# Kernel optimization log

Measured on AMD Instinct MI355X. Metric: run time of the kernel, lower is better.

## Reference

```python
import jax, jax.numpy as jnp
import numpy as np

N_NODES = 262144
D_IN = 256
EMBED_DIM = 256
BATCH_SIZE = 64  # hardcoded in the original module


def setup_inputs() -> dict:
    key = jax.random.key(0)
    k1, k2, k3, k4, k5, k6, k7 = jax.random.split(key, 7)
    nodes = jax.random.normal(k1, (N_NODES, D_IN), dtype=jnp.float32)
    indicator = jnp.sort(jax.random.randint(k2, (N_NODES,), 0, BATCH_SIZE)).astype(jnp.int64)
    mask = jax.random.uniform(k3, (N_NODES,), dtype=jnp.float32)
    # Dense layer params (glorot-like scale)
    scale = 1.0 / np.sqrt(D_IN)
    Wg = jax.random.normal(k4, (D_IN, EMBED_DIM), dtype=jnp.float32) * scale
    bg = jnp.zeros((EMBED_DIM,), dtype=jnp.float32)
    Wf = jax.random.normal(k5, (D_IN, EMBED_DIM), dtype=jnp.float32) * scale
    bf = jnp.zeros((EMBED_DIM,), dtype=jnp.float32)
    return {"nodes": nodes, "indicator": indicator, "mask": mask,
            "Wg": Wg, "bg": bg, "Wf": Wf, "bf": bf}


def reference(nodes, indicator, mask, Wg, bg, Wf, bf):
    seg = indicator.astype(jnp.int32)
    m = mask[:, None]                                   # [N, 1]
    gate = jax.nn.sigmoid(nodes @ Wg + bg)              # [N, E]
    feat = jnp.tanh(nodes @ Wf + bf)                    # [N, E]
    gated_x = gate * feat * m                           # [N, E]
    seg_sum = jax.ops.segment_sum(gated_x, seg, num_segments=BATCH_SIZE)   # [B, E]
    seg_cnt = jax.ops.segment_sum(m, seg, num_segments=BATCH_SIZE)         # [B, 1]
    x_mean = seg_sum / jnp.maximum(seg_cnt, 1e-6)
    x_max = jax.ops.segment_max(gated_x, seg, num_segments=BATCH_SIZE)     # [B, E]
    return jnp.concatenate([x_mean, x_max], axis=-1)    # [B, 2E]
```

## Files before the change

kernel.cpp:

```cpp
#include <hip/hip_runtime.h>
#include <hip/hip_bf16.h>


#define N_NODES 262144
#define BM 64
#define NBLK (N_NODES / BM)

typedef short bf16x8 __attribute__((ext_vector_type(8)));
typedef float f32x4 __attribute__((ext_vector_type(4)));

#define BT_OFF      0
#define SEG_SUM_OFF 262144
#define SEG_MAX_OFF 327680
#define SEG_CNT_OFF 393216

__device__ __forceinline__ unsigned short f2bf(float x) {
    unsigned u = __float_as_uint(x);
    u += 0x7FFFu + ((u >> 16) & 1u);
    return (unsigned short)(u >> 16);
}

__device__ __forceinline__ void atomicMaxF(float* addr, float v) {
    if (v >= 0.0f) atomicMax((int*)addr, __float_as_int(v));
    else           atomicMin((unsigned int*)addr, __float_as_uint(v));
}

__device__ __forceinline__ float fast_sigmoid(float x) {
    return __builtin_amdgcn_rcpf(1.0f + __builtin_amdgcn_exp2f(-1.4426950408889634f * x));
}
__device__ __forceinline__ float fast_tanh(float x) {
    return 1.0f - 2.0f * __builtin_amdgcn_rcpf(1.0f + __builtin_amdgcn_exp2f(2.8853900817779268f * x));
}

__global__ void gr_init(const float* __restrict__ Wg, const float* __restrict__ Wf,
                        unsigned short* __restrict__ Bt, float* __restrict__ seg_sum,
                        float* __restrict__ seg_max, float* __restrict__ seg_cnt) {
    int tid = blockIdx.x * 256 + threadIdx.x;
    int n = tid >> 8, k = tid & 255;
    float v = (n < 256) ? Wg[k * 256 + n] : Wf[k * 256 + (n - 256)];
    Bt[n * 256 + k] = f2bf(v);
    if (tid < 16384) { seg_sum[tid] = 0.0f; seg_max[tid] = __uint_as_float(0xFF800000u); }
    if (tid < 64) seg_cnt[tid] = 0.0f;
}

__global__ __launch_bounds__(512) void gr_main(
    const float* __restrict__ nodes, const int* __restrict__ indicator,
    const float* __restrict__ mask, const float* __restrict__ bg,
    const float* __restrict__ bfb, const unsigned short* __restrict__ Bt,
    float* __restrict__ seg_sum, float* __restrict__ seg_max, float* __restrict__ seg_cnt)
{
    __shared__ unsigned short sA[64 * 264];
    __shared__ unsigned short sB[512 * 40];
    __shared__ float sMask[64];
    __shared__ int sSeg[64];

    const int t = threadIdx.x;
    const long r0 = (long)blockIdx.x * BM;

    #pragma unroll
    for (int i = 0; i < 4; ++i) {
        int c = t + i * 512;
        int row = c >> 5, g = c & 31;
        const float* src = nodes + (r0 + row) * 256 + g * 8;
        float4 f0 = *(const float4*)(src);
        float4 f1 = *(const float4*)(src + 4);
        union { bf16x8 v; unsigned short u[8]; } w;
        w.u[0] = f2bf(f0.x); w.u[1] = f2bf(f0.y); w.u[2] = f2bf(f0.z); w.u[3] = f2bf(f0.w);
        w.u[4] = f2bf(f1.x); w.u[5] = f2bf(f1.y); w.u[6] = f2bf(f1.z); w.u[7] = f2bf(f1.w);
        *reinterpret_cast<bf16x8*>(&sA[row * 264 + g * 8]) = w.v;
    }
    if (t < 64) { sMask[t] = mask[r0 + t]; sSeg[t] = indicator[r0 + t]; }

    const int lane = t & 63, wid = t >> 6;
    const int wr = wid >> 2, wc = wid & 3;
    const int l15 = lane & 15, l4 = lane >> 4;

    f32x4 acc[2][8];
    #pragma unroll
    for (int f = 0; f < 2; ++f)
        #pragma unroll
        for (int n = 0; n < 8; ++n) acc[f][n] = (f32x4){0.f, 0.f, 0.f, 0.f};

    for (int ks = 0; ks < 8; ++ks) {
        __syncthreads();
        #pragma unroll
        for (int i = 0; i < 4; ++i) {
            int c = t + i * 512;
            int n = c >> 2, g = c & 3;
            *reinterpret_cast<bf16x8*>(&sB[n * 40 + g * 8]) =
                *reinterpret_cast<const bf16x8*>(Bt + n * 256 + ks * 32 + g * 8);
        }
        __syncthreads();
        bf16x8 a0 = *reinterpret_cast<const bf16x8*>(&sA[(wr * 32 + l15) * 264 + ks * 32 + l4 * 8]);
        bf16x8 a1 = *reinterpret_cast<const bf16x8*>(&sA[(wr * 32 + 16 + l15) * 264 + ks * 32 + l4 * 8]);
        #pragma unroll
        for (int n = 0; n < 8; ++n) {
            int col = (n < 4) ? (wc * 64 + n * 16) : (256 + wc * 64 + (n - 4) * 16);
            bf16x8 b = *reinterpret_cast<const bf16x8*>(&sB[(col + l15) * 40 + l4 * 8]);
            acc[0][n] = __builtin_amdgcn_mfma_f32_16x16x32_bf16(a0, b, acc[0][n], 0, 0, 0);
            acc[1][n] = __builtin_amdgcn_mfma_f32_16x16x32_bf16(a1, b, acc[1][n], 0, 0, 0);
        }
    }

    const int strip = wr * 32;
    float gated[2][4][4];
    #pragma unroll
    for (int n = 0; n < 4; ++n) {
        int e = wc * 64 + n * 16 + l15;
        float bgv = bg[e], bfv = bfb[e];
        #pragma unroll
        for (int f = 0; f < 2; ++f)
            #pragma unroll
            for (int i = 0; i < 4; ++i) {
                int row = strip + f * 16 + l4 * 4 + i;
                float g = acc[f][n][i] + bgv;
                float h = acc[f][n + 4][i] + bfv;
                gated[f][n][i] = fast_sigmoid(g) * fast_tanh(h) * sMask[row];
            }
    }

    int seg0 = sSeg[strip], seg1 = sSeg[strip + 31];
    if (seg0 == seg1) {
        #pragma unroll
        for (int n = 0; n < 4; ++n) {
            float s = 0.f, m = -3.4e38f;
            #pragma unroll
            for (int f = 0; f < 2; ++f)
                #pragma unroll
                for (int i = 0; i < 4; ++i) {
                    s += gated[f][n][i];
                    m = fmaxf(m, gated[f][n][i]);
                }
            s += __shfl_xor(s, 16); s += __shfl_xor(s, 32);
            m = fmaxf(m, __shfl_xor(m, 16)); m = fmaxf(m, __shfl_xor(m, 32));
            if (l4 == 0) {
                int e = wc * 64 + n * 16 + l15;
                atomicAdd(&seg_sum[seg0 * 256 + e], s);
                atomicMaxF(&seg_max[seg0 * 256 + e], m);
            }
        }
    } else {
        #pragma unroll
        for (int n = 0; n < 4; ++n) {
            int e = wc * 64 + n * 16 + l15;
            #pragma unroll
            for (int f = 0; f < 2; ++f)
                #pragma unroll
                for (int i = 0; i < 4; ++i) {
                    int row = strip + f * 16 + l4 * 4 + i;
                    int sg = sSeg[row];
                    atomicAdd(&seg_sum[sg * 256 + e], gated[f][n][i]);
                    atomicMaxF(&seg_max[sg * 256 + e], gated[f][n][i]);
                }
        }
    }

    if (wid == 0) {
        float mv = sMask[lane];
        if (sSeg[0] == sSeg[63]) {
            float tot = mv;
            #pragma unroll
            for (int off = 1; off < 64; off <<= 1) tot += __shfl_xor(tot, off);
            if (lane == 0) atomicAdd(&seg_cnt[sSeg[0]], tot);
        } else {
            atomicAdd(&seg_cnt[sSeg[lane]], mv);
        }
    }
}

__global__ void gr_final(const float* __restrict__ seg_sum, const float* __restrict__ seg_max,
                         const float* __restrict__ seg_cnt, float* __restrict__ out) {
    int tid = blockIdx.x * 256 + threadIdx.x;
    int s = tid >> 9, j = tid & 511;
    float r;
    if (j < 256) r = seg_sum[s * 256 + j] / fmaxf(seg_cnt[s], 1e-6f);
    else         r = seg_max[s * 256 + (j - 256)];
    out[tid] = r;
}

extern "C" void kernel_launch(void* const* d_in, const int* in_sizes, int n_in,
                              void* d_out, int out_size, void* d_ws, size_t ws_size,
                              hipStream_t stream) {
    const float* nodes     = (const float*)d_in[0];
    const int*   indicator = (const int*)d_in[1];
    const float* mask      = (const float*)d_in[2];
    const float* Wg        = (const float*)d_in[3];
    const float* bg        = (const float*)d_in[4];
    const float* Wf        = (const float*)d_in[5];
    const float* bf        = (const float*)d_in[6];
    float* out = (float*)d_out;

    unsigned short* Bt = (unsigned short*)((char*)d_ws + BT_OFF);
    float* seg_sum = (float*)((char*)d_ws + SEG_SUM_OFF);
    float* seg_max = (float*)((char*)d_ws + SEG_MAX_OFF);
    float* seg_cnt = (float*)((char*)d_ws + SEG_CNT_OFF);

    gr_init<<<512, 256, 0, stream>>>(Wg, Wf, Bt, seg_sum, seg_max, seg_cnt);
    gr_main<<<NBLK, 512, 0, stream>>>(nodes, indicator, mask, bg, bf, Bt,
                                      seg_sum, seg_max, seg_cnt);
    gr_final<<<128, 256, 0, stream>>>(seg_sum, seg_max, seg_cnt, out);
}
```

Measured before the change: 506.1 us.

## Pre-swizzle weights into MFMA fragment layout and load B directly from global

The init kernel now writes the bf16 weights in a fragment-ready layout, transposing through LDS, so each lane of the main kernel can load its B operand with one 16-byte global load per tile. This removes the per-k-step LDS staging of B and the two barriers around it. Each wave now owns 32 output columns across all 64 rows, using a 4x4 MFMA tile instead of 2x8. Launch bounds request two blocks per CU, and mixed-segment tiles get a per-16-row reduction path. The risk is that every block re-reads the 256 KB of weights from L2 and gets less B reuse.

After: 426.3 us. 1.19x faster.

```diff
diff --git a/kernel.cpp b/kernel.cpp
--- a/kernel.cpp
+++ b/kernel.cpp
@@ -33,24 +33,54 @@
 }
 
 __global__ void gr_init(const float* __restrict__ Wg, const float* __restrict__ Wf,
-                        unsigned short* __restrict__ Bt, float* __restrict__ seg_sum,
+                        unsigned short* __restrict__ Btf, float* __restrict__ seg_sum,
                         float* __restrict__ seg_max, float* __restrict__ seg_cnt) {
-    int tid = blockIdx.x * 256 + threadIdx.x;
-    int n = tid >> 8, k = tid & 255;
-    float v = (n < 256) ? Wg[k * 256 + n] : Wf[k * 256 + (n - 256)];
-    Bt[n * 256 + k] = f2bf(v);
-    if (tid < 16384) { seg_sum[tid] = 0.0f; seg_max[tid] = __uint_as_float(0xFF800000u); }
-    if (tid < 64) seg_cnt[tid] = 0.0f;
-}
-
-__global__ __launch_bounds__(512) void gr_main(
+    int b = blockIdx.x;
+    int t = threadIdx.x;
+    if (b >= 32) {
+        int tid = (b - 32) * 256 + t;
+        for (int i = tid; i < 16384; i += 1024) {
+            seg_sum[i] = 0.0f;
+            seg_max[i] = __uint_as_float(0xFF800000u);
+        }
+        if (tid < 64) seg_cnt[tid] = 0.0f;
+        return;
+    }
+    __shared__ float lds[64][68];
+    const int kt  = b >> 3;
+    const int ct0 = (b & 7) * 64;
+    const float* W = (ct0 < 256) ? Wg : Wf;
+    const int cbase = (ct0 < 256) ? ct0 : ct0 - 256;
+    #pragma unroll
+    for (int p = 0; p < 4; ++p) {
+        int kk = (t >> 4) + p * 16;
+        int cc = (t & 15) * 4;
+        float4 v = *(const float4*)(W + (kt * 64 + kk) * 256 + cbase + cc);
+        lds[kk][cc] = v.x; lds[kk][cc + 1] = v.y; lds[kk][cc + 2] = v.z; lds[kk][cc + 3] = v.w;
+    }
+    __syncthreads();
+    #pragma unroll
+    for (int p = 0; p < 2; ++p) {
+        int g = t + p * 256;
+        int lane = g & 63, ksg = (g >> 6) & 1, ct = g >> 7;
+        int cc = ct * 16 + (lane & 15);
+        int kk = ksg * 32 + (lane >> 4) * 8;
+        union { bf16x8 v; unsigned short u[8]; } w;
+        #pragma unroll
+        for (int j = 0; j < 8; ++j) w.u[j] = f2bf(lds[kk + j][cc]);
+        int gct = (ct0 >> 4) + ct;
+        int ks  = kt * 2 + ksg;
+        *reinterpret_cast<bf16x8*>(Btf + (((gct * 8 + ks) * 64 + lane) << 3)) = w.v;
+    }
+}
+
+__global__ __launch_bounds__(512, 2) void gr_main(
     const float* __restrict__ nodes, const int* __restrict__ indicator,
     const float* __restrict__ mask, const float* __restrict__ bg,
-    const float* __restrict__ bfb, const unsigned short* __restrict__ Bt,
+    const float* __restrict__ bfb, const unsigned short* __restrict__ Btf,
     float* __restrict__ seg_sum, float* __restrict__ seg_max, float* __restrict__ seg_cnt)
 {
     __shared__ unsigned short sA[64 * 264];
-    __shared__ unsigned short sB[512 * 40];
     __shared__ float sMask[64];
     __shared__ int sSeg[64];
 
@@ -70,92 +100,109 @@
         *reinterpret_cast<bf16x8*>(&sA[row * 264 + g * 8]) = w.v;
     }
     if (t < 64) { sMask[t] = mask[r0 + t]; sSeg[t] = indicator[r0 + t]; }
-
-    const int lane = t & 63, wid = t >> 6;
-    const int wr = wid >> 2, wc = wid & 3;
+    __syncthreads();
+
+    const int lane = t & 63, wc = t >> 6;
     const int l15 = lane & 15, l4 = lane >> 4;
 
-    f32x4 acc[2][8];
-    #pragma unroll
-    for (int f = 0; f < 2; ++f)
-        #pragma unroll
-        for (int n = 0; n < 8; ++n) acc[f][n] = (f32x4){0.f, 0.f, 0.f, 0.f};
-
+    f32x4 acc[4][4];
+    #pragma unroll
+    for (int m = 0; m < 4; ++m)
+        #pragma unroll
+        for (int n = 0; n < 4; ++n) acc[m][n] = (f32x4){0.f, 0.f, 0.f, 0.f};
+
+    const bf16x8* __restrict__ B8 = (const bf16x8*)Btf;
+    const int tl[4] = { wc * 2, wc * 2 + 1, 16 + wc * 2, 17 + wc * 2 };
+
+    #pragma unroll
     for (int ks = 0; ks < 8; ++ks) {
-        __syncthreads();
-        #pragma unroll
-        for (int i = 0; i < 4; ++i) {
-            int c = t + i * 512;
-            int n = c >> 2, g = c & 3;
-            *reinterpret_cast<bf16x8*>(&sB[n * 40 + g * 8]) =
-                *reinterpret_cast<const bf16x8*>(Bt + n * 256 + ks * 32 + g * 8);
-        }
-        __syncthreads();
-        bf16x8 a0 = *reinterpret_cast<const bf16x8*>(&sA[(wr * 32 + l15) * 264 + ks * 32 + l4 * 8]);
-        bf16x8 a1 = *reinterpret_cast<const bf16x8*>(&sA[(wr * 32 + 16 + l15) * 264 + ks * 32 + l4 * 8]);
-        #pragma unroll
-        for (int n = 0; n < 8; ++n) {
-            int col = (n < 4) ? (wc * 64 + n * 16) : (256 + wc * 64 + (n - 4) * 16);
-            bf16x8 b = *reinterpret_cast<const bf16x8*>(&sB[(col + l15) * 40 + l4 * 8]);
-            acc[0][n] = __builtin_amdgcn_mfma_f32_16x16x32_bf16(a0, b, acc[0][n], 0, 0, 0);
-            acc[1][n] = __builtin_amdgcn_mfma_f32_16x16x32_bf16(a1, b, acc[1][n], 0, 0, 0);
-        }
-    }
-
-    const int strip = wr * 32;
-    float gated[2][4][4];
-    #pragma unroll
-    for (int n = 0; n < 4; ++n) {
-        int e = wc * 64 + n * 16 + l15;
+        bf16x8 b[4];
+        #pragma unroll
+        for (int n = 0; n < 4; ++n) b[n] = B8[(tl[n] * 8 + ks) * 64 + lane];
+        bf16x8 a[4];
+        #pragma unroll
+        for (int m = 0; m < 4; ++m)
+            a[m] = *reinterpret_cast<const bf16x8*>(&sA[(m * 16 + l15) * 264 + ks * 32 + l4 * 8]);
+        #pragma unroll
+        for (int m = 0; m < 4; ++m)
+            #pragma unroll
+            for (int n = 0; n < 4; ++n)
+                acc[m][n] = __builtin_amdgcn_mfma_f32_16x16x32_bf16(a[m], b[n], acc[m][n], 0, 0, 0);
+    }
+
+    float gated[4][2][4];
+    #pragma unroll
+    for (int np = 0; np < 2; ++np) {
+        int e = wc * 32 + np * 16 + l15;
         float bgv = bg[e], bfv = bfb[e];
         #pragma unroll
-        for (int f = 0; f < 2; ++f)
+        for (int m = 0; m < 4; ++m)
             #pragma unroll
             for (int i = 0; i < 4; ++i) {
-                int row = strip + f * 16 + l4 * 4 + i;
-                float g = acc[f][n][i] + bgv;
-                float h = acc[f][n + 4][i] + bfv;
-                gated[f][n][i] = fast_sigmoid(g) * fast_tanh(h) * sMask[row];
+                float g = acc[m][np][i] + bgv;
+                float h = acc[m][np + 2][i] + bfv;
+                gated[m][np][i] = fast_sigmoid(g) * fast_tanh(h) * sMask[m * 16 + l4 * 4 + i];
             }
     }
 
-    int seg0 = sSeg[strip], seg1 = sSeg[strip + 31];
-    if (seg0 == seg1) {
-        #pragma unroll
-        for (int n = 0; n < 4; ++n) {
-            float s = 0.f, m = -3.4e38f;
-            #pragma unroll
-            for (int f = 0; f < 2; ++f)
+    if (sSeg[0] == sSeg[63]) {
+        int sg = sSeg[0];
+        #pragma unroll
+        for (int np = 0; np < 2; ++np) {
+            float s = 0.f, mx = -3.4e38f;
+            #pragma unroll
+            for (int m = 0; m < 4; ++m)
                 #pragma unroll
                 for (int i = 0; i < 4; ++i) {
-                    s += gated[f][n][i];
-                    m = fmaxf(m, gated[f][n][i]);
+                    s += gated[m][np][i];
+                    mx = fmaxf(mx, gated[m][np][i]);
                 }
             s += __shfl_xor(s, 16); s += __shfl_xor(s, 32);
-            m = fmaxf(m, __shfl_xor(m, 16)); m = fmaxf(m, __shfl_xor(m, 32));
+            mx = fmaxf(mx, __shfl_xor(mx, 16)); mx = fmaxf(mx, __shfl_xor(mx, 32));
             if (l4 == 0) {
-                int e = wc * 64 + n * 16 + l15;
-                atomicAdd(&seg_sum[seg0 * 256 + e], s);
-                atomicMaxF(&seg_max[seg0 * 256 + e], m);
+                int e = wc * 32 + np * 16 + l15;
+                atomicAdd(&seg_sum[sg * 256 + e], s);
+                atomicMaxF(&seg_max[sg * 256 + e], mx);
             }
         }
     } else {
         #pragma unroll
-        for (int n = 0; n < 4; ++n) {
-            int e = wc * 64 + n * 16 + l15;
-            #pragma unroll
-            for (int f = 0; f < 2; ++f)
+        for (int m = 0; m < 4; ++m) {
+            int sgA = sSeg[m * 16], sgB = sSeg[m * 16 + 15];
+            if (sgA == sgB) {
                 #pragma unroll
-                for (int i = 0; i < 4; ++i) {
-                    int row = strip + f * 16 + l4 * 4 + i;
-                    int sg = sSeg[row];
-                    atomicAdd(&seg_sum[sg * 256 + e], gated[f][n][i]);
-                    atomicMaxF(&seg_max[sg * 256 + e], gated[f][n][i]);
+                for (int np = 0; np < 2; ++np) {
+                    float s = 0.f, mx = -3.4e38f;
+                    #pragma unroll
+                    for (int i = 0; i < 4; ++i) {
+                        s += gated[m][np][i];
+                        mx = fmaxf(mx, gated[m][np][i]);
+                    }
+                    s += __shfl_xor(s, 16); s += __shfl_xor(s, 32);
+                    mx = fmaxf(mx, __shfl_xor(mx, 16)); mx = fmaxf(mx, __shfl_xor(mx, 32));
+                    if (l4 == 0) {
+                        int e = wc * 32 + np * 16 + l15;
+                        atomicAdd(&seg_sum[sgA * 256 + e], s);
+                        atomicMaxF(&seg_max[sgA * 256 + e], mx);
+                    }
                 }
-        }
-    }
-
-    if (wid == 0) {
+            } else {
+                #pragma unroll
+                for (int np = 0; np < 2; ++np) {
+                    int e = wc * 32 + np * 16 + l15;
+                    #pragma unroll
+                    for (int i = 0; i < 4; ++i) {
+                        int row = m * 16 + l4 * 4 + i;
+                        int sg = sSeg[row];
+                        atomicAdd(&seg_sum[sg * 256 + e], gated[m][np][i]);
+                        atomicMaxF(&seg_max[sg * 256 + e], gated[m][np][i]);
+                    }
+                }
+            }
+        }
+    }
+
+    if (wc == 0) {
         float mv = sMask[lane];
         if (sSeg[0] == sSeg[63]) {
             float tot = mv;
@@ -190,13 +237,13 @@
     const float* bf        = (const float*)d_in[6];
     float* out = (float*)d_out;
 
-    unsigned short* Bt = (unsigned short*)((char*)d_ws + BT_OFF);
+    unsigned short* Btf = (unsigned short*)((char*)d_ws + BT_OFF);
     float* seg_sum = (float*)((char*)d_ws + SEG_SUM_OFF);
     float* seg_max = (float*)((char*)d_ws + SEG_MAX_OFF);
     float* seg_cnt = (float*)((char*)d_ws + SEG_CNT_OFF);
 
-    gr_init<<<512, 256, 0, stream>>>(Wg, Wf, Bt, seg_sum, seg_max, seg_cnt);
-    gr_main<<<NBLK, 512, 0, stream>>>(nodes, indicator, mask, bg, bf, Bt,
+    gr_init<<<36, 256, 0, stream>>>(Wg, Wf, Btf, seg_sum, seg_max, seg_cnt);
+    gr_main<<<NBLK, 512, 0, stream>>>(nodes, indicator, mask, bg, bf, Btf,
                                       seg_sum, seg_max, seg_cnt);
     gr_final<<<128, 256, 0, stream>>>(seg_sum, seg_max, seg_cnt, out);
 }
```
